# Kernel tuning notes

Hardware: AMD Instinct MI355X
Metric: run time of the kernel (lower is better)

## Reference

```python
import jax, jax.numpy as jnp
import numpy as np

N_GAUSSIANS = 512
N_PIXELS = 262144  # 512x512 image


def setup_inputs() -> dict:
    key = jax.random.key(0)
    k1, k2, k3, k4, k5 = jax.random.split(key, 5)
    x = jax.random.uniform(k1, (N_PIXELS, 2), dtype=jnp.float32)
    alphas = (1.0 / N_GAUSSIANS) ** 0.5 * jax.random.uniform(k2, (N_GAUSSIANS, 1), dtype=jnp.float32)
    means = jax.random.uniform(k3, (N_GAUSSIANS, 2), dtype=jnp.float32)
    rotations = jnp.pi * jax.random.uniform(k4, (N_GAUSSIANS, 1), dtype=jnp.float32)
    scales = 0.1 * jax.random.uniform(k5, (N_GAUSSIANS, 2), dtype=jnp.float32)
    return {"x": x, "alphas": alphas, "means": means, "rotations": rotations, "scales": scales}


def _inv2x2(m):
    # m: [N, 2, 2] -> elementwise 2x2 inverse
    a, b = m[:, 0, 0], m[:, 0, 1]
    c, d = m[:, 1, 0], m[:, 1, 1]
    det = a * d - b * c
    inv = jnp.stack([jnp.stack([d, -b], axis=-1),
                     jnp.stack([-c, a], axis=-1)], axis=-2)
    return inv / det[:, None, None]


def reference(x, alphas, means, rotations, scales):
    rot = rotations[:, 0]                       # [N]
    cth, sth = jnp.cos(rot), jnp.sin(rot)
    s0, s1 = scales[:, 0], scales[:, 1]
    # RS = R @ diag(s): [N, 2, 2]
    RS = jnp.stack([s0 * cth, -s1 * sth, s0 * sth, s1 * cth], axis=-1).reshape(-1, 2, 2)
    RSSR = jnp.einsum('nij,nkj->nik', RS, RS)   # RS @ RS^T
    cov = _inv2x2(RSSR)                          # [N, 2, 2]
    rel = x[:, None, :] - means[None, :, :]      # [P, N, 2]
    q = jnp.einsum('pni,nij,pnj->pn', rel, cov, rel)  # quadratic form [P, N]
    g = jnp.exp(-q / 2)                          # [P, N]
    return g @ alphas                            # [P, 1]
```

## Files before the change

### kernel.cpp

```cpp
#include <hip/hip_runtime.h>

#define NG 512
#define NPX 262144
#define BLOCK 256
#define PXPT 2

__global__ __launch_bounds__(BLOCK)
void gsplat_kernel(const float* __restrict__ x,
                   const float* __restrict__ alphas,
                   const float* __restrict__ means,
                   const float* __restrict__ rotations,
                   const float* __restrict__ scales,
                   float* __restrict__ out)
{
    __shared__ float4 gp[NG];
    __shared__ float2 gm[NG];

    for (int n = threadIdx.x; n < NG; n += BLOCK) {
        float rot = rotations[n];
        float sth, cth;
        sincosf(rot, &sth, &cth);
        float s0 = scales[2 * n + 0];
        float s1 = scales[2 * n + 1];
        float r00 = s0 * cth, r01 = -s1 * sth;
        float r10 = s0 * sth, r11 =  s1 * cth;
        float A = r00 * r00 + r01 * r01;
        float B = r00 * r10 + r01 * r11;
        float D = r10 * r10 + r11 * r11;
        float det = A * D - B * B;
        float c00 =  D / det;
        float c01 = -B / det;
        float c11 =  A / det;
        gp[n] = make_float4(c00, 2.0f * c01, c11, alphas[n]);
        gm[n] = make_float2(means[2 * n + 0], means[2 * n + 1]);
    }
    __syncthreads();

    int tid = blockIdx.x * BLOCK + threadIdx.x;
    float4 xv = ((const float4*)x)[tid];
    float x0 = xv.x, y0 = xv.y;
    float x1 = xv.z, y1 = xv.w;

    float acc0 = 0.0f, acc1 = 0.0f;
    #pragma unroll 8
    for (int n = 0; n < NG; ++n) {
        float4 p = gp[n];
        float2 m = gm[n];
        float dx0 = x0 - m.x, dy0 = y0 - m.y;
        float dx1 = x1 - m.x, dy1 = y1 - m.y;
        float q0 = fmaf(p.x * dx0, dx0, fmaf(p.y * dx0, dy0, p.z * dy0 * dy0));
        float q1 = fmaf(p.x * dx1, dx1, fmaf(p.y * dx1, dy1, p.z * dy1 * dy1));
        acc0 = fmaf(p.w, __expf(-0.5f * q0), acc0);
        acc1 = fmaf(p.w, __expf(-0.5f * q1), acc1);
    }

    ((float2*)out)[tid] = make_float2(acc0, acc1);
}

extern "C" void kernel_launch(void* const* d_in, const int* in_sizes, int n_in,
                              void* d_out, int out_size, void* d_ws, size_t ws_size,
                              hipStream_t stream) {
    const float* x         = (const float*)d_in[0];
    const float* alphas    = (const float*)d_in[1];
    const float* means     = (const float*)d_in[2];
    const float* rotations = (const float*)d_in[3];
    const float* scales    = (const float*)d_in[4];
    float* out = (float*)d_out;

    int grid = NPX / (BLOCK * PXPT);
    gsplat_kernel<<<grid, BLOCK, 0, stream>>>(x, alphas, means, rotations, scales, out);
}
```

Measured before the change: 111.4 us.

## Factor Gaussian quadratic form via Cholesky and use native exp2

Each Gaussian's inverse covariance, pre-scaled by log2(e)/2, is factored into a triangular form with the means folded into offsets. The inner loop then computes two affine terms and a sum of squares, and calls the hardware exp2 builtin directly with no scaling multiply. This cuts per-pixel-per-Gaussian ALU work in the hot loop. The change also raises unroll to 16 and adds a min-blocks-per-CU launch bound of 2. Cholesky via sqrt slightly changes rounding but stays valid for positive-definite covariances.

```diff
diff --git a/kernel.cpp b/kernel.cpp
--- a/kernel.cpp
+++ b/kernel.cpp
@@ -5,7 +5,15 @@
 #define BLOCK 256
 #define PXPT 2
 
-__global__ __launch_bounds__(BLOCK)
+#if __has_builtin(__builtin_amdgcn_exp2f)
+  #define KSCALE 0.72134752044448170368f
+  #define EXPNEG(w) __builtin_amdgcn_exp2f(-(w))
+#else
+  #define KSCALE 0.5f
+  #define EXPNEG(w) __expf(-(w))
+#endif
+
+__global__ __launch_bounds__(BLOCK, 2)
 void gsplat_kernel(const float* __restrict__ x,
                    const float* __restrict__ alphas,
                    const float* __restrict__ means,
@@ -13,8 +21,8 @@
                    const float* __restrict__ scales,
                    float* __restrict__ out)
 {
-    __shared__ float4 gp[NG];
-    __shared__ float2 gm[NG];
+    __shared__ float4 ga[NG];
+    __shared__ float2 gb[NG];
 
     for (int n = threadIdx.x; n < NG; n += BLOCK) {
         float rot = rotations[n];
@@ -24,15 +32,21 @@
         float s1 = scales[2 * n + 1];
         float r00 = s0 * cth, r01 = -s1 * sth;
         float r10 = s0 * sth, r11 =  s1 * cth;
-        float A = r00 * r00 + r01 * r01;
-        float B = r00 * r10 + r01 * r11;
-        float D = r10 * r10 + r11 * r11;
-        float det = A * D - B * B;
-        float c00 =  D / det;
-        float c01 = -B / det;
-        float c11 =  A / det;
-        gp[n] = make_float4(c00, 2.0f * c01, c11, alphas[n]);
-        gm[n] = make_float2(means[2 * n + 0], means[2 * n + 1]);
+        float Ar = r00 * r00 + r01 * r01;
+        float Br = r00 * r10 + r01 * r11;
+        float Dr = r10 * r10 + r11 * r11;
+        float det = Ar * Dr - Br * Br;
+        float kc00 =  KSCALE * Dr / det;
+        float kc01 = -KSCALE * Br / det;
+        float p00 = sqrtf(kc00);
+        float p01 = kc01 / p00;
+        float p11 = sqrtf(KSCALE / Dr);
+        float mx = means[2 * n + 0];
+        float my = means[2 * n + 1];
+        float nuoff = -(p00 * mx + p01 * my);
+        float nvoff = -(p11 * my);
+        ga[n] = make_float4(p00, p01, nuoff, alphas[n]);
+        gb[n] = make_float2(p11, nvoff);
     }
     __syncthreads();
 
@@ -42,16 +56,18 @@
     float x1 = xv.z, y1 = xv.w;
 
     float acc0 = 0.0f, acc1 = 0.0f;
-    #pragma unroll 8
+    #pragma unroll 16
     for (int n = 0; n < NG; ++n) {
-        float4 p = gp[n];
-        float2 m = gm[n];
-        float dx0 = x0 - m.x, dy0 = y0 - m.y;
-        float dx1 = x1 - m.x, dy1 = y1 - m.y;
-        float q0 = fmaf(p.x * dx0, dx0, fmaf(p.y * dx0, dy0, p.z * dy0 * dy0));
-        float q1 = fmaf(p.x * dx1, dx1, fmaf(p.y * dx1, dy1, p.z * dy1 * dy1));
-        acc0 = fmaf(p.w, __expf(-0.5f * q0), acc0);
-        acc1 = fmaf(p.w, __expf(-0.5f * q1), acc1);
+        float4 a = ga[n];
+        float2 b = gb[n];
+        float u0 = fmaf(a.x, x0, fmaf(a.y, y0, a.z));
+        float v0 = fmaf(b.x, y0, b.y);
+        float u1 = fmaf(a.x, x1, fmaf(a.y, y1, a.z));
+        float v1 = fmaf(b.x, y1, b.y);
+        float w0 = fmaf(v0, v0, u0 * u0);
+        float w1 = fmaf(v1, v1, u1 * u1);
+        acc0 = fmaf(a.w, EXPNEG(w0), acc0);
+        acc1 = fmaf(a.w, EXPNEG(w1), acc1);
     }
 
     ((float2*)out)[tid] = make_float2(acc0, acc1);
```

After: 98.56 us. 1.13x faster.
